# Performance work log

Measured on AMD Instinct MI355X. Metric: run time of the kernel, lower is better.

The kernel has to match this reference:

```python
import jax, jax.numpy as jnp
import numpy as np

KS = 3          # kernel_size
NUM_FA = 16     # number of functional atoms per pixel
TOTAL_BASES = 6 # num_bases * (ks // 2)
BN_EPS = 1e-5


def _conv3x3(x, w, b):
    # NCHW conv, padding=1, stride=1
    y = jax.lax.conv_general_dilated(
        x, w, window_strides=(1, 1), padding=[(1, 1), (1, 1)],
        dimension_numbers=("NCHW", "OIHW", "NCHW"))
    return y + b[None, :, None, None]


def _bn(x, gamma, beta, mean, var):
    scale = gamma / jnp.sqrt(var + BN_EPS)
    return (x - mean[None, :, None, None]) * scale[None, :, None, None] + beta[None, :, None, None]


def setup_inputs() -> dict:
    key = jax.random.key(0)
    ks = jax.random.split(key, 16)
    N, C, H, W = 16, 64, 64, 64
    INTER, BC_DIM, O = 64, TOTAL_BASES * NUM_FA, 128
    f32 = jnp.float32
    return {
        "x": jax.random.normal(ks[0], (N, C, H, W), f32),
        "conv1_w": jax.random.normal(ks[1], (INTER, C, 3, 3), f32) * 0.05,
        "conv1_b": jax.random.normal(ks[2], (INTER,), f32) * 0.05,
        "bn1_gamma": jax.random.uniform(ks[3], (INTER,), f32, 0.5, 1.5),
        "bn1_beta": jax.random.normal(ks[4], (INTER,), f32) * 0.05,
        "bn1_mean": jax.random.normal(ks[5], (INTER,), f32) * 0.05,
        "bn1_var": jax.random.uniform(ks[6], (INTER,), f32, 0.5, 1.5),
        "conv2_w": jax.random.normal(ks[7], (BC_DIM, INTER, 3, 3), f32) * 0.05,
        "conv2_b": jax.random.normal(ks[8], (BC_DIM,), f32) * 0.05,
        "bn2_gamma": jax.random.uniform(ks[9], (BC_DIM,), f32, 0.5, 1.5),
        "bn2_beta": jax.random.normal(ks[10], (BC_DIM,), f32) * 0.05,
        "bn2_mean": jax.random.normal(ks[11], (BC_DIM,), f32) * 0.05,
        "bn2_var": jax.random.uniform(ks[12], (BC_DIM,), f32, 0.5, 1.5),
        "bases": jax.random.normal(ks[13], (TOTAL_BASES, KS * KS), f32),
        "coef": jax.random.normal(ks[14], (O, C * NUM_FA), f32) * 0.02,
    }


def reference(x, conv1_w, conv1_b, bn1_gamma, bn1_beta, bn1_mean, bn1_var,
              conv2_w, conv2_b, bn2_gamma, bn2_beta, bn2_mean, bn2_var,
              bases, coef):
    N, C, H, W = x.shape
    # bases_net: conv3x3 -> BN -> tanh -> conv3x3 -> BN -> tanh
    h = jnp.tanh(_bn(_conv3x3(x, conv1_w, conv1_b), bn1_gamma, bn1_beta, bn1_mean, bn1_var))
    bc = jnp.tanh(_bn(_conv3x3(h, conv2_w, conv2_b), bn2_gamma, bn2_beta, bn2_mean, bn2_var))
    # torch: .transpose(1,-1).view(N,H,W,num_fa,total_bases)  (swaps H/W; H==W)
    bases_coef = jnp.transpose(bc, (0, 3, 2, 1)).reshape(N, H, W, NUM_FA, TOTAL_BASES)
    # atoms: (bases_coef[...,None] * bases).sum(-2).transpose(-1,-2) -> (N,H,W,ks2,num_fa)
    atoms = jnp.einsum("nhwft,tk->nhwkf", bases_coef, bases)
    # unfold(x, ks, padding=1) -> patches (N,H,W,C,ks2), channel-major like torch unfold
    xp = jnp.pad(x, ((0, 0), (0, 0), (1, 1), (1, 1)))
    patches = jnp.stack([xp[:, :, i:i + H, j:j + W] for i in range(KS) for j in range(KS)], axis=2)  # (N,C,9,H,W)
    patches = jnp.transpose(patches, (0, 3, 4, 1, 2))  # (N,H,W,C,9)
    # (x.unsqueeze(-1) * atoms.unsqueeze(-3)).sum(-2) -> (N,H,W,C,num_fa) -> flatten C-major
    bases_out = jnp.einsum("nhwck,nhwkf->nhwcf", patches, atoms).reshape(N, H, W, C * NUM_FA)
    # torch: .transpose(1,-1) -> (N, C*num_fa, W, H), then 1x1 conv with coef
    out = jnp.einsum("nhwd,od->nowh", bases_out, coef)  # (N, O, W, H)
    return out
```

## Files before the change

kernel.cpp:

```cpp
#include <hip/hip_runtime.h>
#include <math.h>
#include <string.h>

#define NBATCH 16

typedef __attribute__((ext_vector_type(8))) short short8;
typedef __attribute__((ext_vector_type(4))) float floatx4;
#define MFMA16(a, b, c) __builtin_amdgcn_mfma_f32_16x16x32_bf16(a, b, c, 0, 0, 0)

#define GLOAD(dst, ptr, offlit)                                   \
  asm volatile("global_load_dwordx4 %0, %1, off offset:" offlit   \
               : "=&v"(dst)                                       \
               : "v"(ptr)                                         \
               : "memory")

__device__ __forceinline__ unsigned int cvtpk(float a, float b) {
  unsigned int r;
  asm("v_cvt_pk_bf16_f32 %0, %1, %2" : "=v"(r) : "v"(a), "v"(b));
  return r;
}
__device__ __forceinline__ unsigned short f2bf(float f) {
  return (unsigned short)(cvtpk(f, 0.f) & 0xffffu);
}
__device__ __forceinline__ unsigned int packbf2(float a, float b) {
  return cvtpk(a, b);
}
__device__ __forceinline__ float bflo(unsigned int u) {
  return __uint_as_float(u << 16);
}
__device__ __forceinline__ float bfhi(unsigned int u) {
  return __uint_as_float(u & 0xffff0000u);
}
__device__ __forceinline__ float fast_tanh(float x) {
  float e = __expf(2.f * x);
  return 1.f - 2.f / (e + 1.f);
}

__global__ __launch_bounds__(256) void prep_all(
    const float* __restrict__ x, unsigned short* __restrict__ xb,
    const float* __restrict__ w1, const float* __restrict__ w2,
    const float* __restrict__ coef, unsigned short* __restrict__ w1swz,
    unsigned short* __restrict__ w2swz, unsigned short* __restrict__ coefswz) {
  __shared__ float tile[64][65];
  const int t = threadIdx.x;
  if (blockIdx.x < 64) {
    const int y = blockIdx.x, n = blockIdx.y;
    const float* xn = x + (size_t)n * 64 * 4096 + y * 64;
#pragma unroll
    for (int it = 0; it < 16; ++it) {
      int idx = it * 256 + t;
      int c = idx >> 6, xx = idx & 63;
      tile[c][xx] = xn[c * 4096 + xx];
    }
    __syncthreads();
    const int xx = t >> 2, cq = t & 3;
    unsigned short* dst = xb + ((size_t)n * 4096 + y * 64 + xx) * 64;
#pragma unroll
    for (int jj = 0; jj < 2; ++jj) {
      int ch0 = cq * 16 + jj * 8;
      unsigned int p[4];
#pragma unroll
      for (int e = 0; e < 4; ++e)
        p[e] = packbf2(tile[ch0 + e * 2][xx], tile[ch0 + e * 2 + 1][xx]);
      *(uint4*)&dst[ch0] = make_uint4(p[0], p[1], p[2], p[3]);
    }
    return;
  }
  int i = ((blockIdx.x - 64) * NBATCH + blockIdx.y) * 256 + t;
  if (i < 131072) {
    int j = i & 7, f = i >> 3;
    int lane = f & 63;
    int u = (f >> 6) & 3;
    int wj = (f >> 8) & 1;
    int kc = (f >> 9) & 1;
    int rd = f >> 10;
    int lm = lane & 15, lq = lane >> 4;
    int oc = wj * 64 + u * 16 + lm;
    int k = rd * 64 + kc * 32 + lq * 8 + j;
    coefswz[i] = f2bf(coef[oc * 1024 + k]);
  }
  if (i < 36864) {
    int j = i & 7, f = i >> 3;
    int lane = f & 63;
    int u = (f >> 6) & 1;
    int wn = (f >> 7) & 1;
    int kc = (f >> 8) & 1;
    int off = f >> 9;
    int lm = lane & 15, lq = lane >> 4;
    int oc = wn * 32 + u * 16 + lm;
    int ic = kc * 32 + lq * 8 + j;
    w1swz[i] = f2bf(w1[(oc * 64 + ic) * 9 + off]);
  }
  if (i < 55296) {
    int j = i & 7, f = i >> 3;
    int lane = f & 63;
    int rem = f >> 6;
    int u = rem % 3;
    int rem2 = rem / 3;
    int wn = rem2 & 1;
    int kc = (rem2 >> 1) & 1;
    int off = rem2 >> 2;
    int lm = lane & 15, lq = lane >> 4;
    int oc = wn * 48 + u * 16 + lm;
    int ic = kc * 32 + lq * 8 + j;
    w2swz[i] = f2bf(w2[(oc * 64 + ic) * 9 + off]);
  }
}

__global__ __launch_bounds__(256) void fused_conv(
    const unsigned short* __restrict__ xb, const unsigned short* __restrict__ w1swz,
    const unsigned short* __restrict__ w2swz, const float* __restrict__ b1,
    const float* __restrict__ g1, const float* __restrict__ be1,
    const float* __restrict__ m1, const float* __restrict__ v1,
    const float* __restrict__ b2, const float* __restrict__ g2,
    const float* __restrict__ be2, const float* __restrict__ m2,
    const float* __restrict__ v2, unsigned short* __restrict__ bcg) {
  __shared__ unsigned short xls[144 * 72];
  __shared__ unsigned short hls[128 * 72];

  const int t = threadIdx.x;
  const int tile = blockIdx.x, n = blockIdx.y;
  const int x0 = (tile & 7) * 8, y0 = (tile >> 3) * 8;

  const unsigned short* xbn = xb + (size_t)n * 4096 * 64;
#pragma unroll
  for (int it = 0; it < 5; ++it) {
    int idx = it * 256 + t;
    if (idx < 1152) {
      int pos = idx >> 3, u4 = idx & 7;
      int xr = pos / 12, xc = pos - xr * 12;
      int gy = y0 - 2 + xr, gx = x0 - 2 + xc;
      uint4 v = {0u, 0u, 0u, 0u};
      if ((unsigned)gy < 64u && (unsigned)gx < 64u)
        v = *(const uint4*)&xbn[((size_t)gy * 64 + gx) * 64 + u4 * 8];
      *(uint4*)&xls[pos * 72 + u4 * 8] = v;
    }
  }
  __syncthreads();

  const int lane = t & 63, w = t >> 6;
  const int wm = w & 1, wn = w >> 1;
  const int lm = lane & 15, lq = lane >> 4;

  int abase[4];
#pragma unroll
  for (int i = 0; i < 4; ++i) {
    int px = (wm + 2 * i) * 16 + lm;
    if (px > 99) px = 99;
    int hr = px / 10, hc = px - hr * 10;
    abase[i] = (hr * 12 + hc) * 72 + lq * 8;
  }
  floatx4 acc[4][2];
#pragma unroll
  for (int i = 0; i < 4; ++i)
#pragma unroll
    for (int u = 0; u < 2; ++u) acc[i][u] = floatx4{0.f, 0.f, 0.f, 0.f};

#pragma unroll
  for (int step = 0; step < 18; ++step) {
    const int off = step >> 1, kc = step & 1;
    const int di = off / 3, dj = off % 3;
    short8 b[2];
#pragma unroll
    for (int u = 0; u < 2; ++u)
      b[u] = *(const short8*)&w1swz[(off * 512 + kc * 256 + wn * 128 + u * 64 +
                                     lane) * 8];
#pragma unroll
    for (int i = 0; i < 4; ++i) {
      short8 a = *(const short8*)&xls[abase[i] + (di * 12 + dj) * 72 + kc * 32];
      acc[i][0] = MFMA16(a, b[0], acc[i][0]);
      acc[i][1] = MFMA16(a, b[1], acc[i][1]);
    }
  }
  {
    float sc[2], sh[2];
#pragma unroll
    for (int u = 0; u < 2; ++u) {
      int oc = wn * 32 + u * 16 + lm;
      sc[u] = g1[oc] * rsqrtf(v1[oc] + 1e-5f);
      sh[u] = (b1[oc] - m1[oc]) * sc[u] + be1[oc];
    }
#pragma unroll
    for (int i = 0; i < 4; ++i) {
      int px0 = (wm + 2 * i) * 16 + lq * 4;
#pragma unroll
      for (int u = 0; u < 2; ++u) {
        int oc = wn * 32 + u * 16 + lm;
#pragma unroll
        for (int r = 0; r < 4; ++r) {
          int px = px0 + r;
          if (px < 100) {
            int hr = px / 10, hc = px - hr * 10;
            int gy = y0 - 1 + hr, gx = x0 - 1 + hc;
            bool valid = ((unsigned)gy < 64u) && ((unsigned)gx < 64u);
            float val = valid ? fast_tanh(acc[i][u][r] * sc[u] + sh[u]) : 0.f;
            hls[px * 72 + oc] = f2bf(val);
          }
        }
      }
    }
  }
  __syncthreads();

  int hbase[2];
#pragma unroll
  for (int s = 0; s < 2; ++s) {
    int opx = (wm + 2 * s) * 16 + lm;
    int yl = opx >> 3, xl = opx & 7;
    hbase[s] = (yl * 10 + xl) * 72 + lq * 8;
  }
  floatx4 acc2[2][3];
#pragma unroll
  for (int s = 0; s < 2; ++s)
#pragma unroll
    for (int u = 0; u < 3; ++u) acc2[s][u] = floatx4{0.f, 0.f, 0.f, 0.f};

#pragma unroll
  for (int step = 0; step < 18; ++step) {
    const int off = step >> 1, kc = step & 1;
    const int di = off / 3, dj = off % 3;
    short8 b[3];
#pragma unroll
    for (int u = 0; u < 3; ++u)
      b[u] = *(const short8*)&w2swz[(off * 768 + kc * 384 + wn * 192 + u * 64 +
                                     lane) * 8];
#pragma unroll
    for (int s = 0; s < 2; ++s) {
      short8 a = *(const short8*)&hls[hbase[s] + (di * 10 + dj) * 72 + kc * 32];
      acc2[s][0] = MFMA16(a, b[0], acc2[s][0]);
      acc2[s][1] = MFMA16(a, b[1], acc2[s][1]);
      acc2[s][2] = MFMA16(a, b[2], acc2[s][2]);
    }
  }
  {
    float sc[3], sh[3];
#pragma unroll
    for (int u = 0; u < 3; ++u) {
      int oc = wn * 48 + u * 16 + lm;
      sc[u] = g2[oc] * rsqrtf(v2[oc] + 1e-5f);
      sh[u] = (b2[oc] - m2[oc]) * sc[u] + be2[oc];
    }
    unsigned short* bcn = bcg + (size_t)n * 4096 * 96;
#pragma unroll
    for (int s = 0; s < 2; ++s) {
      int opx0 = (wm + 2 * s) * 16 + lq * 4;
#pragma unroll
      for (int u = 0; u < 3; ++u) {
        int oc = wn * 48 + u * 16 + lm;
#pragma unroll
        for (int r = 0; r < 4; ++r) {
          int opx = opx0 + r;
          int y = y0 + (opx >> 3), xx = x0 + (opx & 7);
          bcn[((size_t)y * 64 + xx) * 96 + oc] =
              f2bf(fast_tanh(acc2[s][u][r] * sc[u] + sh[u]));
        }
      }
    }
  }
}

__global__ __launch_bounds__(256, 2) void adconv_final(
    const unsigned short* __restrict__ xb, const unsigned short* __restrict__ bc,
    const float* __restrict__ bases, const unsigned short* __restrict__ coefswz,
    float* __restrict__ out) {
  __shared__ float xs[100 * 68];
  __shared__ unsigned short As[4 * 1024];

  const int t = threadIdx.x;
  const int tile = blockIdx.x, n = blockIdx.y;
  const int q0 = (tile & 7) * 8, p0 = (tile >> 3) * 8;

  float bs[54];
#pragma unroll
  for (int i = 0; i < 54; ++i) bs[i] = bases[i];

  const unsigned short* xbn = xb + (size_t)n * 4096 * 64;
#pragma unroll
  for (int it = 0; it < 4; ++it) {
    int idx = it * 256 + t;
    if (idx < 800) {
      int pos = idx >> 3, u4 = idx & 7;
      int row = pos / 10, col = pos - row * 10;
      int gp = p0 - 1 + row, gq = q0 - 1 + col;
      uint4 v = {0u, 0u, 0u, 0u};
      if ((unsigned)gp < 64u && (unsigned)gq < 64u)
        v = *(const uint4*)&xbn[((size_t)gp * 64 + gq) * 64 + u4 * 8];
      float* d = &xs[pos * 68 + u4 * 8];
      *(float4*)d = make_float4(bflo(v.x), bfhi(v.x), bflo(v.y), bfhi(v.y));
      *(float4*)(d + 4) =
          make_float4(bflo(v.z), bfhi(v.z), bflo(v.w), bfhi(v.w));
    }
  }

  const int lane = t & 63, w = t >> 6;
  const int lm = lane & 15, lq = lane >> 4;

  const int pxl_b = lane >> 2, fh4 = lane & 3;
  const int px_b = w * 16 + pxl_b;
  const int qx_b = px_b >> 3, py_b = px_b & 7;

  float atf[9][4];
  {
    const unsigned short* bp =
        bc + ((size_t)n * 4096 + (q0 + qx_b) * 64 + (p0 + py_b)) * 96 + fh4 * 24;
    float bcv[24];
#pragma unroll
    for (int m = 0; m < 3; ++m) {
      uint4 v = *(const uint4*)(bp + m * 8);
      unsigned int uu[4] = {v.x, v.y, v.z, v.w};
#pragma unroll
      for (int e = 0; e < 4; ++e) {
        bcv[m * 8 + e * 2] = bflo(uu[e]);
        bcv[m * 8 + e * 2 + 1] = bfhi(uu[e]);
      }
    }
#pragma unroll
    for (int j = 0; j < 4; ++j)
#pragma unroll
      for (int k = 0; k < 9; ++k) {
        float s0 = 0.f;
#pragma unroll
        for (int tt = 0; tt < 6; ++tt)
          s0 = fmaf(bcv[j * 6 + tt], bs[tt * 9 + k], s0);
        atf[k][j] = s0;
      }
  }

  int pa[9];
#pragma unroll
  for (int i = 0; i < 3; ++i)
#pragma unroll
    for (int j = 0; j < 3; ++j)
      pa[i * 3 + j] = ((py_b + i) * 10 + qx_b + j) * 68;

  floatx4 acc[2][4];
#pragma unroll
  for (int wj = 0; wj < 2; ++wj)
#pragma unroll
    for (int u = 0; u < 4; ++u) acc[wj][u] = floatx4{0.f, 0.f, 0.f, 0.f};

  unsigned short* Asw = &As[w * 1024];

  float4 qv[9];
  auto qload = [&](int rd) {
    const int coff = rd * 4;
#pragma unroll
    for (int p = 0; p < 9; ++p) qv[p] = *(const float4*)&xs[pa[p] + coff];
  };
  auto build = [&]() {
    float a[4][4];
    {
#pragma unroll
      for (int j = 0; j < 4; ++j) {
        float av = atf[0][j];
        a[0][j] = qv[0].x * av;
        a[1][j] = qv[0].y * av;
        a[2][j] = qv[0].z * av;
        a[3][j] = qv[0].w * av;
      }
    }
#pragma unroll
    for (int p = 1; p < 9; ++p) {
#pragma unroll
      for (int j = 0; j < 4; ++j) {
        float av = atf[p][j];
        a[0][j] = fmaf(qv[p].x, av, a[0][j]);
        a[1][j] = fmaf(qv[p].y, av, a[1][j]);
        a[2][j] = fmaf(qv[p].z, av, a[2][j]);
        a[3][j] = fmaf(qv[p].w, av, a[3][j]);
      }
    }
#pragma unroll
    for (int cc = 0; cc < 4; ++cc) {
      int g = (cc * 4 + fh4) ^ ((pxl_b & 7) << 1);
      uint2 val;
      val.x = cvtpk(a[cc][0], a[cc][1]);
      val.y = cvtpk(a[cc][2], a[cc][3]);
      *(uint2*)&Asw[pxl_b * 64 + g * 4] = val;
    }
  };

  __syncthreads();
  qload(0);
  build();

  for (int rd = 0; rd < 16; ++rd) {
    short8 Bf[2][2][4];
    {
      const unsigned short* b0 = coefswz + (size_t)rd * 8192 + lane * 8;
      const unsigned short* b1 = b0 + 2048;
      const unsigned short* b2 = b0 + 4096;
      const unsigned short* b3 = b0 + 6144;
      GLOAD(Bf[0][0][0], b0, "0");
      GLOAD(Bf[0][0][1], b0, "1024");
      GLOAD(Bf[0][0][2], b0, "2048");
      GLOAD(Bf[0][0][3], b0, "3072");
      GLOAD(Bf[0][1][0], b1, "0");
      GLOAD(Bf[0][1][1], b1, "1024");
      GLOAD(Bf[0][1][2], b1, "2048");
      GLOAD(Bf[0][1][3], b1, "3072");
      GLOAD(Bf[1][0][0], b2, "0");
      GLOAD(Bf[1][0][1], b2, "1024");
      GLOAD(Bf[1][0][2], b2, "2048");
      GLOAD(Bf[1][0][3], b2, "3072");
      GLOAD(Bf[1][1][0], b3, "0");
      GLOAD(Bf[1][1][1], b3, "1024");
      GLOAD(Bf[1][1][2], b3, "2048");
      GLOAD(Bf[1][1][3], b3, "3072");
    }
    short8 Af[2];
#pragma unroll
    for (int kc = 0; kc < 2; ++kc) {
      int u16 = (kc * 4 + lq) ^ (lm & 7);
      Af[kc] = *(const short8*)&Asw[lm * 64 + u16 * 8];
    }
    __builtin_amdgcn_sched_barrier(0);
    if (rd < 15) {
      qload(rd + 1);
      build();
    }
    asm volatile("s_waitcnt vmcnt(0)" ::: "memory");
    __builtin_amdgcn_sched_barrier(0);
    __builtin_amdgcn_s_setprio(1);
#pragma unroll
    for (int kc = 0; kc < 2; ++kc)
#pragma unroll
      for (int wj = 0; wj < 2; ++wj)
#pragma unroll
        for (int u = 0; u < 4; ++u)
          acc[wj][u] = MFMA16(Af[kc], Bf[kc][wj][u], acc[wj][u]);
    __builtin_amdgcn_s_setprio(0);
  }

  float* outn = out + (size_t)n * 128 * 4096;
#pragma unroll
  for (int wj = 0; wj < 2; ++wj)
#pragma unroll
    for (int u = 0; u < 4; ++u) {
      int oc = wj * 64 + u * 16 + lm;
      int gpx = w * 16 + lq * 4;
      int qx = gpx >> 3, py0 = gpx & 7;
      *(float4*)&outn[((size_t)oc * 64 + q0 + qx) * 64 + p0 + py0] =
          make_float4(acc[wj][u][0], acc[wj][u][1], acc[wj][u][2],
                      acc[wj][u][3]);
    }
}

extern "C" void kernel_launch(void* const* d_in, const int* in_sizes, int n_in,
                              void* d_out, int out_size, void* d_ws,
                              size_t ws_size, hipStream_t stream) {
  const float* x = (const float*)d_in[0];
  const float* conv1_w = (const float*)d_in[1];
  const float* conv1_b = (const float*)d_in[2];
  const float* bn1_g = (const float*)d_in[3];
  const float* bn1_b = (const float*)d_in[4];
  const float* bn1_m = (const float*)d_in[5];
  const float* bn1_v = (const float*)d_in[6];
  const float* conv2_w = (const float*)d_in[7];
  const float* conv2_b = (const float*)d_in[8];
  const float* bn2_g = (const float*)d_in[9];
  const float* bn2_b = (const float*)d_in[10];
  const float* bn2_m = (const float*)d_in[11];
  const float* bn2_v = (const float*)d_in[12];
  const float* bases = (const float*)d_in[13];
  const float* coef = (const float*)d_in[14];
  float* out = (float*)d_out;

  char* ws = (char*)d_ws;
  unsigned short* xbuf = (unsigned short*)(ws);
  unsigned short* bcb = (unsigned short*)(ws + 8388608);
  unsigned short* w1swz = (unsigned short*)(ws + 20971520);
  unsigned short* w2swz = (unsigned short*)(ws + 21045248);
  unsigned short* coefswz = (unsigned short*)(ws + 21155840);

  prep_all<<<dim3(96, NBATCH), 256, 0, stream>>>(x, xbuf, conv1_w, conv2_w,
                                                 coef, w1swz, w2swz, coefswz);
  fused_conv<<<dim3(64, NBATCH), 256, 0, stream>>>(
      xbuf, w1swz, w2swz, conv1_b, bn1_g, bn1_b, bn1_m, bn1_v, conv2_b, bn2_g,
      bn2_b, bn2_m, bn2_v, bcb);
  adconv_final<<<dim3(64, NBATCH), 256, 0, stream>>>(xbuf, bcb, bases, coefswz,
                                                     out);
}
```

Before: 162.3 us.

## Fuse bases-net convs and adaptive conv into a single kernel via LDS handoff

Measured after the change: 169.1 us, median of 2. 4.2% more time.

```diff
diff --git a/kernel.cpp b/kernel.cpp
--- a/kernel.cpp
+++ b/kernel.cpp
@@ -107,22 +107,28 @@
   }
 }
 
-__global__ __launch_bounds__(256) void fused_conv(
+__global__ __launch_bounds__(256, 2) void mega(
     const unsigned short* __restrict__ xb, const unsigned short* __restrict__ w1swz,
     const unsigned short* __restrict__ w2swz, const float* __restrict__ b1,
     const float* __restrict__ g1, const float* __restrict__ be1,
     const float* __restrict__ m1, const float* __restrict__ v1,
     const float* __restrict__ b2, const float* __restrict__ g2,
     const float* __restrict__ be2, const float* __restrict__ m2,
-    const float* __restrict__ v2, unsigned short* __restrict__ bcg) {
+    const float* __restrict__ v2, const float* __restrict__ bases,
+    const unsigned short* __restrict__ coefswz, float* __restrict__ out) {
   __shared__ unsigned short xls[144 * 72];
-  __shared__ unsigned short hls[128 * 72];
+  __shared__ unsigned short hls[100 * 72];
+  __shared__ unsigned short lbc[64 * 96];
+  __shared__ unsigned short As[4 * 1024];
+  __shared__ unsigned short xs[100 * 72];
 
   const int t = threadIdx.x;
   const int tile = blockIdx.x, n = blockIdx.y;
   const int x0 = (tile & 7) * 8, y0 = (tile >> 3) * 8;
+  const int q0 = y0, p0 = x0;
 
   const unsigned short* xbn = xb + (size_t)n * 4096 * 64;
+
 #pragma unroll
   for (int it = 0; it < 5; ++it) {
     int idx = it * 256 + t;
@@ -136,43 +142,57 @@
       *(uint4*)&xls[pos * 72 + u4 * 8] = v;
     }
   }
+#pragma unroll
+  for (int it = 0; it < 4; ++it) {
+    int idx = it * 256 + t;
+    if (idx < 800) {
+      int pos = idx >> 3, u4 = idx & 7;
+      int row = pos / 10, col = pos - row * 10;
+      int gp = p0 - 1 + row, gq = q0 - 1 + col;
+      uint4 v = {0u, 0u, 0u, 0u};
+      if ((unsigned)gp < 64u && (unsigned)gq < 64u)
+        v = *(const uint4*)&xbn[((size_t)gp * 64 + gq) * 64 + u4 * 8];
+      *(uint4*)&xs[pos * 72 + u4 * 8] = v;
+    }
+  }
   __syncthreads();
 
   const int lane = t & 63, w = t >> 6;
   const int wm = w & 1, wn = w >> 1;
   const int lm = lane & 15, lq = lane >> 4;
 
-  int abase[4];
-#pragma unroll
-  for (int i = 0; i < 4; ++i) {
-    int px = (wm + 2 * i) * 16 + lm;
-    if (px > 99) px = 99;
-    int hr = px / 10, hc = px - hr * 10;
-    abase[i] = (hr * 12 + hc) * 72 + lq * 8;
-  }
-  floatx4 acc[4][2];
-#pragma unroll
-  for (int i = 0; i < 4; ++i)
-#pragma unroll
-    for (int u = 0; u < 2; ++u) acc[i][u] = floatx4{0.f, 0.f, 0.f, 0.f};
-
-#pragma unroll
-  for (int step = 0; step < 18; ++step) {
-    const int off = step >> 1, kc = step & 1;
-    const int di = off / 3, dj = off % 3;
-    short8 b[2];
-#pragma unroll
-    for (int u = 0; u < 2; ++u)
-      b[u] = *(const short8*)&w1swz[(off * 512 + kc * 256 + wn * 128 + u * 64 +
-                                     lane) * 8];
+  {
+    int abase[4];
 #pragma unroll
     for (int i = 0; i < 4; ++i) {
-      short8 a = *(const short8*)&xls[abase[i] + (di * 12 + dj) * 72 + kc * 32];
-      acc[i][0] = MFMA16(a, b[0], acc[i][0]);
-      acc[i][1] = MFMA16(a, b[1], acc[i][1]);
-    }
-  }
-  {
+      int px = (wm + 2 * i) * 16 + lm;
+      if (px > 99) px = 99;
+      int hr = px / 10, hc = px - hr * 10;
+      abase[i] = (hr * 12 + hc) * 72 + lq * 8;
+    }
+    floatx4 acc[4][2];
+#pragma unroll
+    for (int i = 0; i < 4; ++i)
+#pragma unroll
+      for (int u = 0; u < 2; ++u) acc[i][u] = floatx4{0.f, 0.f, 0.f, 0.f};
+
+#pragma unroll
+    for (int step = 0; step < 18; ++step) {
+      const int off = step >> 1, kc = step & 1;
+      const int di = off / 3, dj = off % 3;
+      short8 b[2];
+#pragma unroll
+      for (int u = 0; u < 2; ++u)
+        b[u] = *(const short8*)&w1swz[(off * 512 + kc * 256 + wn * 128 +
+                                       u * 64 + lane) * 8];
+#pragma unroll
+      for (int i = 0; i < 4; ++i) {
+        short8 a =
+            *(const short8*)&xls[abase[i] + (di * 12 + dj) * 72 + kc * 32];
+        acc[i][0] = MFMA16(a, b[0], acc[i][0]);
+        acc[i][1] = MFMA16(a, b[1], acc[i][1]);
+      }
+    }
     float sc[2], sh[2];
 #pragma unroll
     for (int u = 0; u < 2; ++u) {
@@ -202,37 +222,38 @@
   }
   __syncthreads();
 
-  int hbase[2];
-#pragma unroll
-  for (int s = 0; s < 2; ++s) {
-    int opx = (wm + 2 * s) * 16 + lm;
-    int yl = opx >> 3, xl = opx & 7;
-    hbase[s] = (yl * 10 + xl) * 72 + lq * 8;
-  }
-  floatx4 acc2[2][3];
-#pragma unroll
-  for (int s = 0; s < 2; ++s)
-#pragma unroll
-    for (int u = 0; u < 3; ++u) acc2[s][u] = floatx4{0.f, 0.f, 0.f, 0.f};
-
-#pragma unroll
-  for (int step = 0; step < 18; ++step) {
-    const int off = step >> 1, kc = step & 1;
-    const int di = off / 3, dj = off % 3;
-    short8 b[3];
-#pragma unroll
-    for (int u = 0; u < 3; ++u)
-      b[u] = *(const short8*)&w2swz[(off * 768 + kc * 384 + wn * 192 + u * 64 +
-                                     lane) * 8];
+  {
+    int hbase[2];
 #pragma unroll
     for (int s = 0; s < 2; ++s) {
-      short8 a = *(const short8*)&hls[hbase[s] + (di * 10 + dj) * 72 + kc * 32];
-      acc2[s][0] = MFMA16(a, b[0], acc2[s][0]);
-      acc2[s][1] = MFMA16(a, b[1], acc2[s][1]);
-      acc2[s][2] = MFMA16(a, b[2], acc2[s][2]);
-    }
-  }
-  {
+      int opx = (wm + 2 * s) * 16 + lm;
+      int yl = opx >> 3, xl = opx & 7;
+      hbase[s] = (yl * 10 + xl) * 72 + lq * 8;
+    }
+    floatx4 acc2[2][3];
+#pragma unroll
+    for (int s = 0; s < 2; ++s)
+#pragma unroll
+      for (int u = 0; u < 3; ++u) acc2[s][u] = floatx4{0.f, 0.f, 0.f, 0.f};
+
+#pragma unroll
+    for (int step = 0; step < 18; ++step) {
+      const int off = step >> 1, kc = step & 1;
+      const int di = off / 3, dj = off % 3;
+      short8 b[3];
+#pragma unroll
+      for (int u = 0; u < 3; ++u)
+        b[u] = *(const short8*)&w2swz[(off * 768 + kc * 384 + wn * 192 +
+                                       u * 64 + lane) * 8];
+#pragma unroll
+      for (int s = 0; s < 2; ++s) {
+        short8 a =
+            *(const short8*)&hls[hbase[s] + (di * 10 + dj) * 72 + kc * 32];
+        acc2[s][0] = MFMA16(a, b[0], acc2[s][0]);
+        acc2[s][1] = MFMA16(a, b[1], acc2[s][1]);
+        acc2[s][2] = MFMA16(a, b[2], acc2[s][2]);
+      }
+    }
     float sc[3], sh[3];
 #pragma unroll
     for (int u = 0; u < 3; ++u) {
@@ -240,7 +261,6 @@
       sc[u] = g2[oc] * rsqrtf(v2[oc] + 1e-5f);
       sh[u] = (b2[oc] - m2[oc]) * sc[u] + be2[oc];
     }
-    unsigned short* bcn = bcg + (size_t)n * 4096 * 96;
 #pragma unroll
     for (int s = 0; s < 2; ++s) {
       int opx0 = (wm + 2 * s) * 16 + lq * 4;
@@ -250,50 +270,16 @@
 #pragma unroll
         for (int r = 0; r < 4; ++r) {
           int opx = opx0 + r;
-          int y = y0 + (opx >> 3), xx = x0 + (opx & 7);
-          bcn[((size_t)y * 64 + xx) * 96 + oc] =
-              f2bf(fast_tanh(acc2[s][u][r] * sc[u] + sh[u]));
+          lbc[opx * 96 + oc] = f2bf(fast_tanh(acc2[s][u][r] * sc[u] + sh[u]));
         }
       }
     }
   }
-}
-
-__global__ __launch_bounds__(256, 2) void adconv_final(
-    const unsigned short* __restrict__ xb, const unsigned short* __restrict__ bc,
-    const float* __restrict__ bases, const unsigned short* __restrict__ coefswz,
-    float* __restrict__ out) {
-  __shared__ float xs[100 * 68];
-  __shared__ unsigned short As[4 * 1024];
-
-  const int t = threadIdx.x;
-  const int tile = blockIdx.x, n = blockIdx.y;
-  const int q0 = (tile & 7) * 8, p0 = (tile >> 3) * 8;
+  __syncthreads();
 
   float bs[54];
 #pragma unroll
   for (int i = 0; i < 54; ++i) bs[i] = bases[i];
-
-  const unsigned short* xbn = xb + (size_t)n * 4096 * 64;
-#pragma unroll
-  for (int it = 0; it < 4; ++it) {
-    int idx = it * 256 + t;
-    if (idx < 800) {
-      int pos = idx >> 3, u4 = idx & 7;
-      int row = pos / 10, col = pos - row * 10;
-      int gp = p0 - 1 + row, gq = q0 - 1 + col;
-      uint4 v = {0u, 0u, 0u, 0u};
-      if ((unsigned)gp < 64u && (unsigned)gq < 64u)
-        v = *(const uint4*)&xbn[((size_t)gp * 64 + gq) * 64 + u4 * 8];
-      float* d = &xs[pos * 68 + u4 * 8];
-      *(float4*)d = make_float4(bflo(v.x), bfhi(v.x), bflo(v.y), bfhi(v.y));
-      *(float4*)(d + 4) =
-          make_float4(bflo(v.z), bfhi(v.z), bflo(v.w), bfhi(v.w));
-    }
-  }
-
-  const int lane = t & 63, w = t >> 6;
-  const int lm = lane & 15, lq = lane >> 4;
 
   const int pxl_b = lane >> 2, fh4 = lane & 3;
   const int px_b = w * 16 + pxl_b;
@@ -301,8 +287,7 @@
 
   float atf[9][4];
   {
-    const unsigned short* bp =
-        bc + ((size_t)n * 4096 + (q0 + qx_b) * 64 + (p0 + py_b)) * 96 + fh4 * 24;
+    const unsigned short* bp = &lbc[px_b * 96 + fh4 * 24];
     float bcv[24];
 #pragma unroll
     for (int m = 0; m < 3; ++m) {
@@ -331,7 +316,7 @@
   for (int i = 0; i < 3; ++i)
 #pragma unroll
     for (int j = 0; j < 3; ++j)
-      pa[i * 3 + j] = ((py_b + i) * 10 + qx_b + j) * 68;
+      pa[i * 3 + j] = ((py_b + i) * 10 + qx_b + j) * 72;
 
   floatx4 acc[2][4];
 #pragma unroll
@@ -341,33 +326,37 @@
 
   unsigned short* Asw = &As[w * 1024];
 
-  float4 qv[9];
+  uint2 qv[9];
   auto qload = [&](int rd) {
     const int coff = rd * 4;
 #pragma unroll
-    for (int p = 0; p < 9; ++p) qv[p] = *(const float4*)&xs[pa[p] + coff];
+    for (int p = 0; p < 9; ++p) qv[p] = *(const uint2*)&xs[pa[p] + coff];
   };
   auto build = [&]() {
     float a[4][4];
     {
+      float c0 = bflo(qv[0].x), c1 = bfhi(qv[0].x);
+      float c2 = bflo(qv[0].y), c3 = bfhi(qv[0].y);
 #pragma unroll
       for (int j = 0; j < 4; ++j) {
         float av = atf[0][j];
-        a[0][j] = qv[0].x * av;
-        a[1][j] = qv[0].y * av;
-        a[2][j] = qv[0].z * av;
-        a[3][j] = qv[0].w * av;
+        a[0][j] = c0 * av;
+        a[1][j] = c1 * av;
+        a[2][j] = c2 * av;
+        a[3][j] = c3 * av;
       }
     }
 #pragma unroll
     for (int p = 1; p < 9; ++p) {
+      float c0 = bflo(qv[p].x), c1 = bfhi(qv[p].x);
+      float c2 = bflo(qv[p].y), c3 = bfhi(qv[p].y);
 #pragma unroll
       for (int j = 0; j < 4; ++j) {
         float av = atf[p][j];
-        a[0][j] = fmaf(qv[p].x, av, a[0][j]);
-        a[1][j] = fmaf(qv[p].y, av, a[1][j]);
-        a[2][j] = fmaf(qv[p].z, av, a[2][j]);
-        a[3][j] = fmaf(qv[p].w, av, a[3][j]);
+        a[0][j] = fmaf(c0, av, a[0][j]);
+        a[1][j] = fmaf(c1, av, a[1][j]);
+        a[2][j] = fmaf(c2, av, a[2][j]);
+        a[3][j] = fmaf(c3, av, a[3][j]);
       }
     }
 #pragma unroll
@@ -380,7 +369,6 @@
     }
   };
 
-  __syncthreads();
   qload(0);
   build();
 
@@ -468,16 +456,13 @@
 
   char* ws = (char*)d_ws;
   unsigned short* xbuf = (unsigned short*)(ws);
-  unsigned short* bcb = (unsigned short*)(ws + 8388608);
   unsigned short* w1swz = (unsigned short*)(ws + 20971520);
   unsigned short* w2swz = (unsigned short*)(ws + 21045248);
   unsigned short* coefswz = (unsigned short*)(ws + 21155840);
 
   prep_all<<<dim3(96, NBATCH), 256, 0, stream>>>(x, xbuf, conv1_w, conv2_w,
                                                  coef, w1swz, w2swz, coefswz);
-  fused_conv<<<dim3(64, NBATCH), 256, 0, stream>>>(
+  mega<<<dim3(64, NBATCH), 256, 0, stream>>>(
       xbuf, w1swz, w2swz, conv1_b, bn1_g, bn1_b, bn1_m, bn1_v, conv2_b, bn2_g,
-      bn2_b, bn2_m, bn2_v, bcb);
-  adconv_final<<<dim3(64, NBATCH), 256, 0, stream>>>(xbuf, bcb, bases, coefswz,
-                                                     out);
-}
+      bn2_b, bn2_m, bn2_v, bases, coefswz, out);
+}
```
